# Optimization experiments

Measured on AMD Instinct MI355X. Metric: run time of the kernel, lower is better.

The kernel has to match this reference:

```python
import jax, jax.numpy as jnp
import numpy as np

B, C, Z, H, W = 16, 1, 1, 512, 512
N_ITER = 128
STEP = 0.97 / 3.0  # 0.97 / stacked_operator_norm, used for both primal and dual stepsizes
DIMS = (-2, -1)


def _fft2c(x):
    # MRpro FastFourierOp convention: centered orthonormal FFT
    return jnp.fft.fftshift(jnp.fft.fftn(jnp.fft.ifftshift(x, DIMS), axes=DIMS, norm='ortho'), DIMS)


def _ifft2c(k):
    return jnp.fft.fftshift(jnp.fft.ifftn(jnp.fft.ifftshift(k, DIMS), axes=DIMS, norm='ortho'), DIMS)


def _fgrad(x):
    # forward finite differences with circular padding, stacked along a new leading dim
    return jnp.stack([jnp.roll(x, -1, axis=d) - x for d in DIMS], axis=0)


def _fgrad_adj(p):
    # adjoint of forward circular difference: backward difference (negative divergence)
    return sum(jnp.roll(p[i], 1, axis=d) - p[i] for i, d in enumerate(DIMS))


def setup_inputs() -> dict:
    key = jax.random.key(0)
    k1, k2, k3, k4, k5, k6 = jax.random.split(key, 6)
    shape = (B, C, Z, H, W)
    initial_image_r = jax.random.normal(k1, shape, jnp.float32)
    initial_image_i = jax.random.normal(k2, shape, jnp.float32)
    kdata_r = jax.random.normal(k3, shape, jnp.float32)
    kdata_i = jax.random.normal(k4, shape, jnp.float32)
    mask = jax.random.randint(k5, (1, 1, 1, H, W), 0, 2).astype(jnp.int32)
    # strictly positive spatially adaptive regularization parameter map
    lam = jax.random.uniform(k6, shape, jnp.float32, minval=1e-3, maxval=0.1)
    return {'initial_image_r': initial_image_r, 'initial_image_i': initial_image_i,
            'kdata_r': kdata_r, 'kdata_i': kdata_i, 'lam': lam, 'mask': mask}


def reference(initial_image_r, initial_image_i, kdata_r, kdata_i, lam, mask):
    x = jax.lax.complex(initial_image_r, initial_image_i)
    y = jax.lax.complex(kdata_r, kdata_i)
    m = mask.astype(jnp.float32)
    sigma = jnp.float32(STEP)
    tau = jnp.float32(STEP)

    p1 = jnp.zeros_like(y)                      # dual for data term (k-space shape)
    p2 = jnp.zeros((2,) + x.shape, x.dtype)     # dual for TV term (2 gradient components)
    xbar = x

    def body(carry, _):
        x, xbar, p1, p2 = carry
        # dual ascent + prox of conjugates
        p1 = p1 + sigma * (m * _fft2c(xbar))
        p1 = (p1 - sigma * y) / (1.0 + sigma)          # prox_{sigma f1*}, f1 = 0.5||.-y||^2
        q = p2 + sigma * _fgrad(xbar)
        # prox_{sigma f2*}, f2 = ||lam .||_1 viewed as real: clamp real & imag to [-lam, lam]
        p2 = jax.lax.complex(jnp.clip(q.real, -lam, lam), jnp.clip(q.imag, -lam, lam))
        # primal descent (g = 0 so prox is identity) + extrapolation (theta = 1)
        x_new = x - tau * (_ifft2c(m * p1) + _fgrad_adj(p2))
        xbar = 2.0 * x_new - x
        return (x_new, xbar, p1, p2), None

    (x, xbar, p1, p2), _ = jax.lax.scan(body, (x, xbar, p1, p2), None, length=N_ITER)
    # return complex solution as stacked (real, imag) float tensor
    return jnp.stack((x.real, x.imag), axis=-1)
```

## Files before the change

### kernel.cpp

```cpp
#include <hip/hip_runtime.h>
#include <hip/hip_fp16.h>
#include <cstddef>

#define NBATCH 16
#define NSIDE  512
#define NT     (NBATCH * NSIDE * NSIDE)
#define NLINES 8
#define LSTRIDE 577
#define APACK  (512 * 512)

constexpr float SIGMA = (float)(0.97 / 3.0);
constexpr float TAU   = (float)(0.97 / 3.0);
constexpr float INV1S = (float)(1.0 / (1.0 + 0.97 / 3.0));
constexpr float INV_N = 1.0f / 512.0f;

__device__ __forceinline__ float2 cadd(float2 a, float2 b){ return make_float2(a.x+b.x, a.y+b.y); }
__device__ __forceinline__ float2 csub(float2 a, float2 b){ return make_float2(a.x-b.x, a.y-b.y); }
__device__ __forceinline__ float2 cmul(float2 a, float2 b){ return make_float2(a.x*b.x - a.y*b.y, a.x*b.y + a.y*b.x); }

__device__ __forceinline__ int SL(int s){ return s + (s >> 3); }
__device__ __forceinline__ int rev9(int s){ return ((s & 7) << 6) | (s & 56) | (s >> 6); }

__device__ __forceinline__ unsigned h2bits(float2 v){
  __half2 h = __floats2half2_rn(v.x, v.y);
  return *reinterpret_cast<unsigned*>(&h);
}
__device__ __forceinline__ float2 bits2f(unsigned u){
  __half2 h = *reinterpret_cast<__half2*>(&u);
  return __half22float2(h);
}

template<int S>
__device__ __forceinline__ void dft8(float2 v[8]){
  const float RS = 0.70710678118654752440f;
  float2 a0 = cadd(v[0], v[4]), a4 = csub(v[0], v[4]);
  float2 a1 = cadd(v[1], v[5]), a5 = csub(v[1], v[5]);
  float2 a2 = cadd(v[2], v[6]), a6 = csub(v[2], v[6]);
  float2 a3 = cadd(v[3], v[7]), a7 = csub(v[3], v[7]);
  a5 = cmul(a5, make_float2(RS, (float)S * RS));
  a6 = make_float2(-(float)S * a6.y, (float)S * a6.x);
  a7 = cmul(a7, make_float2(-RS, (float)S * RS));
  float2 b0 = cadd(a0, a2), b2 = csub(a0, a2);
  float2 b1 = cadd(a1, a3), b3 = csub(a1, a3);
  b3 = make_float2(-(float)S * b3.y, (float)S * b3.x);
  v[0] = cadd(b0, b1); v[4] = csub(b0, b1);
  v[2] = cadd(b2, b3); v[6] = csub(b2, b3);
  float2 c0 = cadd(a4, a6), c2 = csub(a4, a6);
  float2 c1 = cadd(a5, a7), c3 = csub(a5, a7);
  c3 = make_float2(-(float)S * c3.y, (float)S * c3.x);
  v[1] = cadd(c0, c1); v[5] = csub(c0, c1);
  v[3] = cadd(c2, c3); v[7] = csub(c2, c3);
}

__device__ __forceinline__ void fft_fwd_pair(float2* __restrict__ A, float2* __restrict__ B, int l){
  float2 va[8], vb[8];
  #pragma unroll
  for(int j = 0; j < 8; j++){ int s = SL(l + 64*j); va[j] = A[s]; vb[j] = B[s]; }
  dft8<-1>(va); dft8<-1>(vb);
  #pragma unroll
  for(int t = 1; t < 8; t++){
    float sn, cs;
    __sincosf((-6.283185307179586f / 512.0f) * (float)(l * t), &sn, &cs);
    float2 w = make_float2(cs, sn);
    va[t] = cmul(va[t], w); vb[t] = cmul(vb[t], w);
  }
  #pragma unroll
  for(int t = 0; t < 8; t++){ int s = SL(t*64 + l); A[s] = va[t]; B[s] = vb[t]; }
  __syncthreads();
  int tg = l >> 3, m = l & 7;
  #pragma unroll
  for(int j = 0; j < 8; j++){ int s = SL(tg*64 + m + 8*j); va[j] = A[s]; vb[j] = B[s]; }
  dft8<-1>(va); dft8<-1>(vb);
  #pragma unroll
  for(int t = 1; t < 8; t++){
    float sn, cs;
    __sincosf((-6.283185307179586f / 64.0f) * (float)(m * t), &sn, &cs);
    float2 w = make_float2(cs, sn);
    va[t] = cmul(va[t], w); vb[t] = cmul(vb[t], w);
  }
  #pragma unroll
  for(int t = 0; t < 8; t++){ int s = SL(tg*64 + t*8 + m); A[s] = va[t]; B[s] = vb[t]; }
  __syncthreads();
  #pragma unroll
  for(int j = 0; j < 8; j++){ int s = SL(8*l + j); va[j] = A[s]; vb[j] = B[s]; }
  dft8<-1>(va); dft8<-1>(vb);
  #pragma unroll
  for(int t = 0; t < 8; t++){ int s = SL(8*l + t); A[s] = va[t]; B[s] = vb[t]; }
}

__device__ __forceinline__ void fft_inv_pair(float2* __restrict__ A, float2* __restrict__ B, int l){
  float2 va[8], vb[8];
  #pragma unroll
  for(int j = 0; j < 8; j++){ int s = SL(8*l + j); va[j] = A[s]; vb[j] = B[s]; }
  dft8<1>(va); dft8<1>(vb);
  #pragma unroll
  for(int t = 0; t < 8; t++){ int s = SL(8*l + t); A[s] = va[t]; B[s] = vb[t]; }
  __syncthreads();
  int tg = l >> 3, m = l & 7;
  #pragma unroll
  for(int j = 0; j < 8; j++){ int s = SL(tg*64 + 8*j + m); va[j] = A[s]; vb[j] = B[s]; }
  #pragma unroll
  for(int j = 1; j < 8; j++){
    float sn, cs;
    __sincosf((6.283185307179586f / 64.0f) * (float)(m * j), &sn, &cs);
    float2 w = make_float2(cs, sn);
    va[j] = cmul(va[j], w); vb[j] = cmul(vb[j], w);
  }
  dft8<1>(va); dft8<1>(vb);
  #pragma unroll
  for(int j = 0; j < 8; j++){ int s = SL(tg*64 + m + 8*j); A[s] = va[j]; B[s] = vb[j]; }
  __syncthreads();
  #pragma unroll
  for(int t = 0; t < 8; t++){ int s = SL(t*64 + l); va[t] = A[s]; vb[t] = B[s]; }
  #pragma unroll
  for(int t = 1; t < 8; t++){
    float sn, cs;
    __sincosf((6.283185307179586f / 512.0f) * (float)(l * t), &sn, &cs);
    float2 w = make_float2(cs, sn);
    va[t] = cmul(va[t], w); vb[t] = cmul(vb[t], w);
  }
  dft8<1>(va); dft8<1>(vb);
  #pragma unroll
  for(int j = 0; j < 8; j++){ int s = SL(l + 64*j); A[s] = va[j]; B[s] = vb[j]; }
}

__device__ __forceinline__ void store_strip_blk(const float2* __restrict__ lds, __half2* __restrict__ tile, int t){
  int q = t & 3, s0v = t >> 2;
  #pragma unroll
  for(int k = 0; k < 8; k++){
    int s = s0v + 64 * k;
    float2 v0 = lds[(2*q)   * LSTRIDE + SL(s)];
    float2 v1 = lds[(2*q+1) * LSTRIDE + SL(s)];
    uint2 u; u.x = h2bits(v0); u.y = h2bits(v1);
    *reinterpret_cast<uint2*>(tile + s*8 + 2*q) = u;
  }
}

__device__ __forceinline__ void load_strip_blk(float2* __restrict__ lds, const __half2* __restrict__ base,
                                               int lineBase, int t){
  #pragma unroll
  for(int k = 0; k < 4; k++){
    int idx = t + 256 * k;
    int tb = idx >> 4;
    int rem = idx & 15;
    int g = rem >> 1, h = rem & 1;
    uint4 u = *reinterpret_cast<const uint4*>(base + ((size_t)tb << 12) + ((lineBase + g) << 3) + (h << 2));
    int n = (tb << 3) + (h << 2);
    lds[g * LSTRIDE + SL(n)]     = bits2f(u.x);
    lds[g * LSTRIDE + SL(n + 1)] = bits2f(u.y);
    lds[g * LSTRIDE + SL(n + 2)] = bits2f(u.z);
    lds[g * LSTRIDE + SL(n + 3)] = bits2f(u.w);
  }
}

__global__ __launch_bounds__(256) void k_fwd_rows(const float* __restrict__ ir, const float* __restrict__ ii,
                                                  __half2* __restrict__ U){
  __shared__ float2 lds[NLINES * LSTRIDE];
  int b = blockIdx.x >> 6, rb = blockIdx.x & 63, r0 = rb << 3;
  int t = threadIdx.x;
  int rr = t >> 5, col = t & 31;
  size_t base = ((size_t)(b * 512 + r0 + rr) << 9);
  #pragma unroll
  for(int k = 0; k < 16; k++){
    int c = col + 32 * k;
    float sc = ((r0 + rr + c) & 1) ? -INV_N : INV_N;
    lds[rr * LSTRIDE + SL(c)] = make_float2(sc * ir[base + c], sc * ii[base + c]);
  }
  __syncthreads();
  int wv = t >> 6, l = t & 63;
  fft_fwd_pair(&lds[wv * LSTRIDE], &lds[(wv + 4) * LSTRIDE], l);
  __syncthreads();
  store_strip_blk(lds, U + ((size_t)(b * 64 + rb) << 12), t);
}

__global__ __launch_bounds__(256) void k_colsA(const __half2* __restrict__ U, __half2* __restrict__ p1p,
                                               const __half2* __restrict__ yp, const int* __restrict__ idx,
                                               const int* __restrict__ cnt, __half2* __restrict__ V,
                                               const __half2* __restrict__ xbarh, __half2* __restrict__ p2h,
                                               __half2* __restrict__ p2w, const __half* __restrict__ lamh){
  __shared__ float2 lds[NLINES * LSTRIDE];
  int b = blockIdx.x >> 6, cb = blockIdx.x & 63, cs0 = cb << 3;
  int t = threadIdx.x;
  int rr = t >> 5, col = t & 31;
  load_strip_blk(lds, U + ((size_t)b << 18), cs0, t);
  __syncthreads();
  int wv = t >> 6, l = t & 63;
  fft_fwd_pair(&lds[wv * LSTRIDE], &lds[(wv + 4) * LSTRIDE], l);
  __syncthreads();
  int g = rr, lane = col;
  int cs = cs0 + g;
  int jbase = cs << 9;
  int jcnt = cnt[cs];
  size_t boff = (size_t)b * APACK;
  int ksi[16]; float2 pn[16];
  #pragma unroll
  for(int tt = 0; tt < 16; tt++){
    int jj = lane + 32 * tt;
    bool act = jj < jcnt;
    int j = jbase + (act ? jj : 0);
    int ks = act ? idx[j] : 0;
    float2 K = lds[g * LSTRIDE + SL(ks)];
    float2 yv = __half22float2(yp[boff + j]);
    float2 p  = __half22float2(p1p[boff + j]);
    float2 v;
    v.x = (p.x + SIGMA * (K.x - yv.x)) * INV1S;
    v.y = (p.y + SIGMA * (K.y - yv.y)) * INV1S;
    if(act) p1p[boff + j] = __floats2half2_rn(v.x, v.y);
    ksi[tt] = act ? ks : -1;
    pn[tt] = v;
  }
  __syncthreads();
  #pragma unroll
  for(int k = 0; k < 16; k++) lds[rr * LSTRIDE + SL(col + 32 * k)] = make_float2(0.0f, 0.0f);
  __syncthreads();
  #pragma unroll
  for(int tt = 0; tt < 16; tt++) if(ksi[tt] >= 0) lds[g * LSTRIDE + SL(ksi[tt])] = pn[tt];
  __syncthreads();
  fft_inv_pair(&lds[wv * LSTRIDE], &lds[(wv + 4) * LSTRIDE], l);
  __syncthreads();
  store_strip_blk(lds, V + ((size_t)(b * 64 + cb) << 12), t);

  int base_i = blockIdx.x << 12;
  #pragma unroll
  for(int k = 0; k < 16; k++){
    int i = base_i + (k << 8) + t;
    int c = i & 511, r = (i >> 9) & 511;
    int idn = (r < 511) ? i + 512 : i - (511 << 9);
    int irt = (c < 511) ? i + 1   : i - 511;
    float2 xc = __half22float2(xbarh[i]);
    float2 xd = __half22float2(xbarh[idn]);
    float2 xr = __half22float2(xbarh[irt]);
    float lv = __half2float(lamh[i]);
    float2 qh = __half22float2(p2h[i]);
    float2 qw = __half22float2(p2w[i]);
    qh.x += SIGMA * (xd.x - xc.x); qh.y += SIGMA * (xd.y - xc.y);
    qw.x += SIGMA * (xr.x - xc.x); qw.y += SIGMA * (xr.y - xc.y);
    qh.x = fminf(fmaxf(qh.x, -lv), lv); qh.y = fminf(fmaxf(qh.y, -lv), lv);
    qw.x = fminf(fmaxf(qw.x, -lv), lv); qw.y = fminf(fmaxf(qw.y, -lv), lv);
    p2h[i] = __floats2half2_rn(qh.x, qh.y);
    p2w[i] = __floats2half2_rn(qw.x, qw.y);
  }
}

__global__ __launch_bounds__(256) void k_megaB(const __half2* __restrict__ V, const __half2* __restrict__ p2h,
                                               const __half2* __restrict__ p2w, float2* __restrict__ x,
                                               __half2* __restrict__ xbarh, __half2* __restrict__ U, int last){
  __shared__ float2 lds[NLINES * LSTRIDE];
  int b = blockIdx.x >> 6, rb = blockIdx.x & 63, r0 = rb << 3;
  int t = threadIdx.x;
  int rr = t >> 5, col = t & 31;
  load_strip_blk(lds, V + ((size_t)b << 18), r0, t);
  __syncthreads();
  int wv = t >> 6, l = t & 63;
  fft_inv_pair(&lds[wv * LSTRIDE], &lds[(wv + 4) * LSTRIDE], l);
  __syncthreads();
  int r = r0 + rr;
  size_t base   = ((size_t)(b * 512 + r) << 9);
  size_t baseUp = ((size_t)(b * 512 + ((r - 1) & 511)) << 9);
  #pragma unroll
  for(int k = 0; k < 16; k++){
    int c = col + 32 * k;
    int cl = (c - 1) & 511;
    float2 v = lds[rr * LSTRIDE + SL(c)];
    float sc = ((r + c) & 1) ? -INV_N : INV_N;
    float2 ph  = __half22float2(p2h[base + c]);
    float2 phu = __half22float2(p2h[baseUp + c]);
    float2 pw  = __half22float2(p2w[base + c]);
    float2 pwl = __half22float2(p2w[base + cl]);
    float gx = sc * v.x + (phu.x - ph.x) + (pwl.x - pw.x);
    float gy = sc * v.y + (phu.y - ph.y) + (pwl.y - pw.y);
    float2 xo = x[base + c];
    float2 xn = make_float2(xo.x - TAU * gx, xo.y - TAU * gy);
    x[base + c] = xn;
    float2 xb2 = make_float2(2.0f * xn.x - xo.x, 2.0f * xn.y - xo.y);
    xbarh[base + c] = __floats2half2_rn(xb2.x, xb2.y);
    lds[rr * LSTRIDE + SL(c)] = make_float2(sc * xb2.x, sc * xb2.y);
  }
  if(last) return;
  __syncthreads();
  fft_fwd_pair(&lds[wv * LSTRIDE], &lds[(wv + 4) * LSTRIDE], l);
  __syncthreads();
  store_strip_blk(lds, U + ((size_t)(b * 64 + rb) << 12), t);
}

__global__ __launch_bounds__(256) void k_init_x(const float* __restrict__ ir, const float* __restrict__ ii,
                                                float2* __restrict__ x, __half2* __restrict__ xbarh){
  int i = blockIdx.x * 256 + threadIdx.x;
  float vr = ir[i], vi = ii[i];
  x[i] = make_float2(vr, vi);
  xbarh[i] = __floats2half2_rn(vr, vi);
}

__global__ __launch_bounds__(256) void k_init_lam(const float* __restrict__ lam, __half* __restrict__ lamh){
  int i = blockIdx.x * 256 + threadIdx.x;
  lamh[i] = __float2half(lam[i]);
}

__global__ __launch_bounds__(256) void k_pack(const int* __restrict__ mask, const float* __restrict__ kr,
                                              const float* __restrict__ ki, int* __restrict__ idx,
                                              int* __restrict__ cnt, __half2* __restrict__ yp){
  __shared__ int wcnt[8];
  int cs = blockIdx.x;
  int t = threadIdx.x, lane = t & 63, wv = t >> 6;
  int csr = rev9(cs);
  int jbase = cs << 9;
  #pragma unroll
  for(int rnd = 0; rnd < 2; rnd++){
    int ks = t + 256 * rnd;
    int ksr = rev9(ks);
    int pred = (mask[(ksr << 9) + csr] != 0) ? 1 : 0;
    unsigned long long bal = __ballot(pred);
    if(lane == 0) wcnt[4 * rnd + wv] = (int)__popcll(bal);
    __syncthreads();
    int pre = 0;
    for(int w = 0; w < wv; w++) pre += wcnt[4 * rnd + w];
    int roundbase = (rnd == 1) ? (wcnt[0] + wcnt[1] + wcnt[2] + wcnt[3]) : 0;
    int lpre = (int)__popcll(bal & ((1ull << lane) - 1ull));
    if(pred){
      int pos = jbase + roundbase + pre + lpre;
      idx[pos] = ks;
      float s = ((ksr + csr) & 1) ? -1.0f : 1.0f;
      for(int b = 0; b < 16; b++){
        size_t a = ((size_t)b << 18) + ((size_t)ksr << 9) + csr;
        yp[(size_t)b * APACK + pos] = __floats2half2_rn(s * kr[a], s * ki[a]);
      }
    }
    __syncthreads();
  }
  if(t == 0) cnt[cs] = wcnt[0] + wcnt[1] + wcnt[2] + wcnt[3] + wcnt[4] + wcnt[5] + wcnt[6] + wcnt[7];
}

extern "C" void kernel_launch(void* const* d_in, const int* in_sizes, int n_in,
                              void* d_out, int out_size, void* d_ws, size_t ws_size,
                              hipStream_t stream){
  const float* ir  = (const float*)d_in[0];
  const float* ii  = (const float*)d_in[1];
  const float* kdr = (const float*)d_in[2];
  const float* kdi = (const float*)d_in[3];
  const float* lam = (const float*)d_in[4];
  const int*  mask = (const int*)d_in[5];
  float2* x = (float2*)d_out;

  char* ws = (char*)d_ws;
  __half2* p1p   = (__half2*)ws;
  __half2* yp    = p1p + (size_t)APACK * 16;
  __half2* p2h   = yp  + (size_t)APACK * 16;
  __half2* p2w   = p2h + NT;
  __half2* U     = p2w + NT;
  __half2* V     = U   + NT;
  __half2* xbarh = V   + NT;
  __half*  lamh  = (__half*)(xbarh + NT);
  int*     idx   = (int*)(lamh + NT);
  int*     cnt   = idx + APACK;

  hipMemsetAsync(p1p, 0, (size_t)APACK * 16 * sizeof(__half2), stream);
  hipMemsetAsync(p2h, 0, (size_t)2 * NT * sizeof(__half2), stream);
  k_pack<<<512, 256, 0, stream>>>(mask, kdr, kdi, idx, cnt, yp);
  k_init_lam<<<NT / 256, 256, 0, stream>>>(lam, lamh);
  k_init_x<<<NT / 256, 256, 0, stream>>>(ir, ii, x, xbarh);
  k_fwd_rows<<<1024, 256, 0, stream>>>(ir, ii, U);

  for(int it = 0; it < 128; it++){
    k_colsA<<<1024, 256, 0, stream>>>(U, p1p, yp, idx, cnt, V, xbarh, p2h, p2w, lamh);
    k_megaB<<<1024, 256, 0, stream>>>(V, p2h, p2w, x, xbarh, U, it == 127 ? 1 : 0);
  }
}
```

Baseline: 7.307 ms.

## Fuse TV dual update into primal kernel with ping-pong buffers and fp16 x

Moves the TV dual ascent and clamp out of the column kernel and into the row-wise primal kernel. Each thread recomputes its own and its up/left neighbours' updated duals from a stencil on xbar, and double-buffers p2 and xbar so reads and writes do not race. This takes the dual pass off the column kernel and removes one round trip of p2 traffic. The primal iterate x is now kept in fp16 rather than fp32 to halve its bandwidth, with fp32 written out only on the last iteration. In exchange it does redundant neighbour computation and extra stencil loads, and it risks accuracy loss from accumulating x in half precision.

Result: no change. 7.312 ms (+0.1%).

```diff
diff --git a/kernel.cpp b/kernel.cpp
--- a/kernel.cpp
+++ b/kernel.cpp
@@ -28,6 +28,9 @@
 __device__ __forceinline__ float2 bits2f(unsigned u){
   __half2 h = *reinterpret_cast<__half2*>(&u);
   return __half22float2(h);
+}
+__device__ __forceinline__ float2 clip2(float2 q, float lv){
+  return make_float2(fminf(fmaxf(q.x, -lv), lv), fminf(fmaxf(q.y, -lv), lv));
 }
 
 template<int S>
@@ -175,9 +178,7 @@
 
 __global__ __launch_bounds__(256) void k_colsA(const __half2* __restrict__ U, __half2* __restrict__ p1p,
                                                const __half2* __restrict__ yp, const int* __restrict__ idx,
-                                               const int* __restrict__ cnt, __half2* __restrict__ V,
-                                               const __half2* __restrict__ xbarh, __half2* __restrict__ p2h,
-                                               __half2* __restrict__ p2w, const __half* __restrict__ lamh){
+                                               const int* __restrict__ cnt, __half2* __restrict__ V){
   __shared__ float2 lds[NLINES * LSTRIDE];
   int b = blockIdx.x >> 6, cb = blockIdx.x & 63, cs0 = cb << 3;
   int t = threadIdx.x;
@@ -219,32 +220,14 @@
   fft_inv_pair(&lds[wv * LSTRIDE], &lds[(wv + 4) * LSTRIDE], l);
   __syncthreads();
   store_strip_blk(lds, V + ((size_t)(b * 64 + cb) << 12), t);
-
-  int base_i = blockIdx.x << 12;
-  #pragma unroll
-  for(int k = 0; k < 16; k++){
-    int i = base_i + (k << 8) + t;
-    int c = i & 511, r = (i >> 9) & 511;
-    int idn = (r < 511) ? i + 512 : i - (511 << 9);
-    int irt = (c < 511) ? i + 1   : i - 511;
-    float2 xc = __half22float2(xbarh[i]);
-    float2 xd = __half22float2(xbarh[idn]);
-    float2 xr = __half22float2(xbarh[irt]);
-    float lv = __half2float(lamh[i]);
-    float2 qh = __half22float2(p2h[i]);
-    float2 qw = __half22float2(p2w[i]);
-    qh.x += SIGMA * (xd.x - xc.x); qh.y += SIGMA * (xd.y - xc.y);
-    qw.x += SIGMA * (xr.x - xc.x); qw.y += SIGMA * (xr.y - xc.y);
-    qh.x = fminf(fmaxf(qh.x, -lv), lv); qh.y = fminf(fmaxf(qh.y, -lv), lv);
-    qw.x = fminf(fmaxf(qw.x, -lv), lv); qw.y = fminf(fmaxf(qw.y, -lv), lv);
-    p2h[i] = __floats2half2_rn(qh.x, qh.y);
-    p2w[i] = __floats2half2_rn(qw.x, qw.y);
-  }
-}
-
-__global__ __launch_bounds__(256) void k_megaB(const __half2* __restrict__ V, const __half2* __restrict__ p2h,
-                                               const __half2* __restrict__ p2w, float2* __restrict__ x,
-                                               __half2* __restrict__ xbarh, __half2* __restrict__ U, int last){
+}
+
+__global__ __launch_bounds__(256) void k_megaB(const __half2* __restrict__ V,
+                                               const __half2* __restrict__ p2h_s, const __half2* __restrict__ p2w_s,
+                                               __half2* __restrict__ p2h_d, __half2* __restrict__ p2w_d,
+                                               const __half2* __restrict__ xb_s, __half2* __restrict__ xb_d,
+                                               __half2* __restrict__ xh, const __half* __restrict__ lamh,
+                                               __half2* __restrict__ U, float2* __restrict__ xout, int last){
   __shared__ float2 lds[NLINES * LSTRIDE];
   int b = blockIdx.x >> 6, rb = blockIdx.x & 63, r0 = rb << 3;
   int t = threadIdx.x;
@@ -255,25 +238,53 @@
   fft_inv_pair(&lds[wv * LSTRIDE], &lds[(wv + 4) * LSTRIDE], l);
   __syncthreads();
   int r = r0 + rr;
-  size_t base   = ((size_t)(b * 512 + r) << 9);
-  size_t baseUp = ((size_t)(b * 512 + ((r - 1) & 511)) << 9);
+  size_t ibase = ((size_t)(b * 512 + r) << 9);
+  size_t ibUp  = ((size_t)(b * 512 + ((r - 1) & 511)) << 9);
+  size_t ibDn  = ((size_t)(b * 512 + ((r + 1) & 511)) << 9);
   #pragma unroll
   for(int k = 0; k < 16; k++){
     int c = col + 32 * k;
-    int cl = (c - 1) & 511;
+    int cl = (c - 1) & 511, cr = (c + 1) & 511;
+    float2 xc = __half22float2(xb_s[ibase + c]);
+    float2 xR = __half22float2(xb_s[ibase + cr]);
+    float2 xL = __half22float2(xb_s[ibase + cl]);
+    float2 xU = __half22float2(xb_s[ibUp + c]);
+    float2 xD = __half22float2(xb_s[ibDn + c]);
+    float lv  = __half2float(lamh[ibase + c]);
+    float lvU = __half2float(lamh[ibUp + c]);
+    float lvL = __half2float(lamh[ibase + cl]);
+    float2 hn  = clip2(make_float2(0,0), 0);
+    {
+      float2 ho = __half22float2(p2h_s[ibase + c]);
+      hn = clip2(make_float2(ho.x + SIGMA * (xD.x - xc.x), ho.y + SIGMA * (xD.y - xc.y)), lv);
+    }
+    float2 hUn;
+    {
+      float2 hu = __half22float2(p2h_s[ibUp + c]);
+      hUn = clip2(make_float2(hu.x + SIGMA * (xc.x - xU.x), hu.y + SIGMA * (xc.y - xU.y)), lvU);
+    }
+    float2 wn;
+    {
+      float2 wo = __half22float2(p2w_s[ibase + c]);
+      wn = clip2(make_float2(wo.x + SIGMA * (xR.x - xc.x), wo.y + SIGMA * (xR.y - xc.y)), lv);
+    }
+    float2 wLn;
+    {
+      float2 wl = __half22float2(p2w_s[ibase + cl]);
+      wLn = clip2(make_float2(wl.x + SIGMA * (xc.x - xL.x), wl.y + SIGMA * (xc.y - xL.y)), lvL);
+    }
+    p2h_d[ibase + c] = __floats2half2_rn(hn.x, hn.y);
+    p2w_d[ibase + c] = __floats2half2_rn(wn.x, wn.y);
     float2 v = lds[rr * LSTRIDE + SL(c)];
     float sc = ((r + c) & 1) ? -INV_N : INV_N;
-    float2 ph  = __half22float2(p2h[base + c]);
-    float2 phu = __half22float2(p2h[baseUp + c]);
-    float2 pw  = __half22float2(p2w[base + c]);
-    float2 pwl = __half22float2(p2w[base + cl]);
-    float gx = sc * v.x + (phu.x - ph.x) + (pwl.x - pw.x);
-    float gy = sc * v.y + (phu.y - ph.y) + (pwl.y - pw.y);
-    float2 xo = x[base + c];
+    float gx = sc * v.x + (hUn.x - hn.x) + (wLn.x - wn.x);
+    float gy = sc * v.y + (hUn.y - hn.y) + (wLn.y - wn.y);
+    float2 xo = __half22float2(xh[ibase + c]);
     float2 xn = make_float2(xo.x - TAU * gx, xo.y - TAU * gy);
-    x[base + c] = xn;
+    xh[ibase + c] = __floats2half2_rn(xn.x, xn.y);
     float2 xb2 = make_float2(2.0f * xn.x - xo.x, 2.0f * xn.y - xo.y);
-    xbarh[base + c] = __floats2half2_rn(xb2.x, xb2.y);
+    xb_d[ibase + c] = __floats2half2_rn(xb2.x, xb2.y);
+    if(last) xout[ibase + c] = xn;
     lds[rr * LSTRIDE + SL(c)] = make_float2(sc * xb2.x, sc * xb2.y);
   }
   if(last) return;
@@ -284,11 +295,10 @@
 }
 
 __global__ __launch_bounds__(256) void k_init_x(const float* __restrict__ ir, const float* __restrict__ ii,
-                                                float2* __restrict__ x, __half2* __restrict__ xbarh){
+                                                __half2* __restrict__ xh, __half2* __restrict__ xb0){
   int i = blockIdx.x * 256 + threadIdx.x;
-  float vr = ir[i], vi = ii[i];
-  x[i] = make_float2(vr, vi);
-  xbarh[i] = __floats2half2_rn(vr, vi);
+  __half2 v = __floats2half2_rn(ir[i], ii[i]);
+  xh[i] = v; xb0[i] = v;
 }
 
 __global__ __launch_bounds__(256) void k_init_lam(const float* __restrict__ lam, __half* __restrict__ lamh){
@@ -344,24 +354,34 @@
   char* ws = (char*)d_ws;
   __half2* p1p   = (__half2*)ws;
   __half2* yp    = p1p + (size_t)APACK * 16;
-  __half2* p2h   = yp  + (size_t)APACK * 16;
-  __half2* p2w   = p2h + NT;
-  __half2* U     = p2w + NT;
+  __half2* p2h0  = yp  + (size_t)APACK * 16;
+  __half2* p2w0  = p2h0 + NT;
+  __half2* p2h1  = p2w0 + NT;
+  __half2* p2w1  = p2h1 + NT;
+  __half2* xb0   = p2w1 + NT;
+  __half2* xb1   = xb0 + NT;
+  __half2* xh    = xb1 + NT;
+  __half2* U     = xh  + NT;
   __half2* V     = U   + NT;
-  __half2* xbarh = V   + NT;
-  __half*  lamh  = (__half*)(xbarh + NT);
+  __half*  lamh  = (__half*)(V + NT);
   int*     idx   = (int*)(lamh + NT);
   int*     cnt   = idx + APACK;
 
   hipMemsetAsync(p1p, 0, (size_t)APACK * 16 * sizeof(__half2), stream);
-  hipMemsetAsync(p2h, 0, (size_t)2 * NT * sizeof(__half2), stream);
+  hipMemsetAsync(p2h0, 0, (size_t)2 * NT * sizeof(__half2), stream);
   k_pack<<<512, 256, 0, stream>>>(mask, kdr, kdi, idx, cnt, yp);
   k_init_lam<<<NT / 256, 256, 0, stream>>>(lam, lamh);
-  k_init_x<<<NT / 256, 256, 0, stream>>>(ir, ii, x, xbarh);
+  k_init_x<<<NT / 256, 256, 0, stream>>>(ir, ii, xh, xb0);
   k_fwd_rows<<<1024, 256, 0, stream>>>(ir, ii, U);
 
+  __half2* p2hs[2] = {p2h0, p2h1};
+  __half2* p2ws[2] = {p2w0, p2w1};
+  __half2* xbs[2]  = {xb0, xb1};
+
   for(int it = 0; it < 128; it++){
-    k_colsA<<<1024, 256, 0, stream>>>(U, p1p, yp, idx, cnt, V, xbarh, p2h, p2w, lamh);
-    k_megaB<<<1024, 256, 0, stream>>>(V, p2h, p2w, x, xbarh, U, it == 127 ? 1 : 0);
-  }
-}
+    int s = it & 1, d = s ^ 1;
+    k_colsA<<<1024, 256, 0, stream>>>(U, p1p, yp, idx, cnt, V);
+    k_megaB<<<1024, 256, 0, stream>>>(V, p2hs[s], p2ws[s], p2hs[d], p2ws[d],
+                                      xbs[s], xbs[d], xh, lamh, U, x, it == 127 ? 1 : 0);
+  }
+}
```
